# Optimization experiments

Measured on AMD Instinct MI355X. Metric: run time of the kernel, lower is better.

The kernel has to match this reference:

```python
import jax, jax.numpy as jnp
import numpy as np
from jax import lax

BN_EPS = 1e-5


def fps(xyz, n_group):
    """Farthest point sampling. xyz: (B,N,3) -> indices (B,n_group)."""
    B, N, _ = xyz.shape

    def step(carry, _):
        dist, far = carry                                   # (B,N), (B,)
        c = jnp.take_along_axis(xyz, far[:, None, None], axis=1)  # (B,1,3)
        d = jnp.sum((xyz - c) ** 2, axis=-1)                # (B,N)
        dist = jnp.minimum(dist, d)
        return (dist, jnp.argmax(dist, axis=-1).astype(jnp.int32)), far

    init = (jnp.full((B, N), 1e10, xyz.dtype), jnp.zeros((B,), jnp.int32))
    _, idxs = lax.scan(step, init, None, length=n_group)
    return jnp.swapaxes(idxs, 0, 1)                         # (B,n_group)


def knn_point(k, xyz, center):
    """k nearest neighbors of each center in xyz. -> idx (B,G,k)."""
    # squared distances (B,G,N), expanded-cdist form
    d = (jnp.sum(center ** 2, -1)[:, :, None]
         + jnp.sum(xyz ** 2, -1)[:, None, :]
         - 2.0 * jnp.einsum('bgc,bnc->bgn', center, xyz))
    _, idx = lax.top_k(-d, k)                               # smallest distances
    return idx


def batchnorm(x, gamma, beta):
    """Training-mode BatchNorm1d over (M, n) per channel. x: (M,n,C)."""
    mu = jnp.mean(x, axis=(0, 1))
    var = jnp.var(x, axis=(0, 1))
    return (x - mu) * lax.rsqrt(var + BN_EPS) * gamma + beta


def encoder(pg, W1, b1, g1, be1, W2, b2, W3, b3, g2, be2, W4, b4):
    """PointNet encoder. pg: (B,G,n,3) -> (B,G,C)."""
    B, G, n, _ = pg.shape
    x = pg.reshape(B * G, n, 3)
    f = jnp.einsum('mnc,oc->mno', x, W1) + b1               # (M,n,128)
    f = jax.nn.relu(batchnorm(f, g1, be1))
    f = jnp.einsum('mnc,oc->mno', f, W2) + b2               # (M,n,256)
    fg = jnp.max(f, axis=1, keepdims=True)                  # (M,1,256)
    f = jnp.concatenate([jnp.broadcast_to(fg, f.shape), f], axis=-1)  # (M,n,512)
    f = jnp.einsum('mnc,oc->mno', f, W3) + b3               # (M,n,512)
    f = jax.nn.relu(batchnorm(f, g2, be2))
    f = jnp.einsum('mnc,oc->mno', f, W4) + b4               # (M,n,C)
    return jnp.max(f, axis=1).reshape(B, G, -1)


def setup_inputs() -> dict:
    key = jax.random.key(0)
    ks = jax.random.split(key, 8)
    C = 128
    xyz = jax.random.normal(ks[0], (16, 8192, 3), jnp.float32)
    s = 0.02
    return {
        'xyz': xyz,
        'W1': jax.random.normal(ks[1], (128, 3), jnp.float32) * s,
        'b1': jnp.zeros((128,), jnp.float32),
        'g1': jnp.ones((128,), jnp.float32),
        'be1': jnp.zeros((128,), jnp.float32),
        'W2': jax.random.normal(ks[2], (256, 128), jnp.float32) * s,
        'b2': jnp.zeros((256,), jnp.float32),
        'W3': jax.random.normal(ks[3], (512, 512), jnp.float32) * s,
        'b3': jnp.zeros((512,), jnp.float32),
        'g2': jnp.ones((512,), jnp.float32),
        'be2': jnp.zeros((512,), jnp.float32),
        'W4': jax.random.normal(ks[4], (C, 512), jnp.float32) * s,
        'b4': jnp.zeros((C,), jnp.float32),
        'n_group': 512,
    }


def reference(xyz, W1, b1, g1, be1, W2, b2, W3, b3, g2, be2, W4, b4, n_group):
    k = 32
    B, N, _ = xyz.shape
    cidx = fps(xyz, n_group)                                # (B,G)
    center = jnp.take_along_axis(xyz, cidx[:, :, None], axis=1)  # (B,G,3)
    idx = knn_point(k, xyz, center)                         # (B,G,k)
    # gather neighborhoods
    neighborhood = jnp.take_along_axis(
        xyz, idx.reshape(B, n_group * k)[:, :, None], axis=1
    ).reshape(B, n_group, k, 3)
    features = encoder(neighborhood, W1, b1, g1, be1, W2, b2, W3, b3, g2, be2, W4, b4)
    return center, features
```

## Files before the change

kernel.cpp:

```cpp
#include <hip/hip_runtime.h>

typedef unsigned short ushortT;
typedef unsigned int uintT;
typedef unsigned long long u64T;
typedef __bf16 bf16x8 __attribute__((ext_vector_type(8)));
typedef float f32x4 __attribute__((ext_vector_type(4)));

#define B_ 16
#define N_ 8192
#define G_ 512
#define KNN_ 32
#define M_ (B_*G_)
#define R_ (M_*KNN_)

static __device__ __forceinline__ ushortT f2bf(float f){
  uintT u = __float_as_uint(f);
  return (ushortT)((u + 0x7fffu + ((u >> 16) & 1u)) >> 16);
}
static __device__ __forceinline__ float bf2f(ushortT h){ return __uint_as_float(((uintT)h) << 16); }

union U16 { uint4 u; ushortT s[8]; bf16x8 v; };

#define SWZ_MAX(vv, pat) {                                              \
    uintT lo_ = (uintT)(vv), hi_ = (uintT)((vv) >> 32);                 \
    uintT olo_ = (uintT)__builtin_amdgcn_ds_swizzle((int)lo_, (pat));   \
    uintT ohi_ = (uintT)__builtin_amdgcn_ds_swizzle((int)hi_, (pat));   \
    u64T o_ = ((u64T)ohi_ << 32) | olo_;                                \
    (vv) = (o_ > (vv)) ? o_ : (vv); }

__global__ __launch_bounds__(512) void fps_kernel(const float* __restrict__ xyz,
                                                  float* __restrict__ center){
  const int b = blockIdx.x;
  const int tid = threadIdx.x;
  const float* P = xyz + (size_t)b * N_ * 3;
  __shared__ float sx[N_], sy[N_], sz[N_];
  __shared__ u64T slot[2][8];
  float px[16], py[16], pz[16], dist[16];
  uintT nI[16];
#pragma unroll
  for (int k = 0; k < 16; k++){
    int p = tid + (k << 9);
    float x = P[p*3+0], y = P[p*3+1], z = P[p*3+2];
    sx[p] = x; sy[p] = y; sz[p] = z;
    px[k] = x; py[k] = y; pz[k] = z;
    dist[k] = 1e10f;
    nI[k] = ~(uintT)p;
  }
  __syncthreads();
  const int lane = tid & 63, wv = tid >> 6;
  int far = 0;
  for (int s = 0; s < G_; s++){
    const float cx = sx[far], cy = sy[far], cz = sz[far];
    if (tid == 0){
      float* co = center + ((size_t)b * G_ + s) * 3;
      co[0] = cx; co[1] = cy; co[2] = cz;
    }
    u64T pk[16];
#pragma unroll
    for (int k = 0; k < 16; k++){
      float d0 = __fsub_rn(px[k], cx), d1 = __fsub_rn(py[k], cy), d2 = __fsub_rn(pz[k], cz);
      float d  = __fadd_rn(__fadd_rn(__fmul_rn(d0,d0), __fmul_rn(d1,d1)), __fmul_rn(d2,d2));
      float dd = fminf(dist[k], d);
      dist[k] = dd;
      pk[k] = ((u64T)__float_as_uint(dd) << 32) | nI[k];
    }
#pragma unroll
    for (int st = 8; st >= 1; st >>= 1)
#pragma unroll
      for (int k = 0; k < st; k++)
        pk[k] = (pk[k + st] > pk[k]) ? pk[k + st] : pk[k];
    u64T best = pk[0];
    SWZ_MAX(best, 0x041F)
    SWZ_MAX(best, 0x081F)
    SWZ_MAX(best, 0x101F)
    SWZ_MAX(best, 0x201F)
    SWZ_MAX(best, 0x401F)
    {
      u64T o = __shfl_xor(best, 32);
      best = (o > best) ? o : best;
    }
    if (lane == 0) slot[s & 1][wv] = best;
    __syncthreads();
    u64T v = slot[s & 1][lane & 7];
    SWZ_MAX(v, 0x041F)
    SWZ_MAX(v, 0x081F)
    SWZ_MAX(v, 0x101F)
    far = (int)(~(uintT)v) & (N_ - 1);
  }
}

__global__ __launch_bounds__(256) void knn_kernel(const float* __restrict__ xyz,
                                                  const float* __restrict__ center,
                                                  int* __restrict__ knnIdx){
  const int mc = blockIdx.x;
  const int b  = mc >> 9;
  const int tid = threadIdx.x;
  const int lane = tid & 63, w = tid >> 6;
  const float* P = xyz + (size_t)b * N_ * 3;
  const float cx = center[mc*3+0], cy = center[mc*3+1], cz = center[mc*3+2];
  const float tc = __fadd_rn(__fadd_rn(__fmul_rn(cx,cx), __fmul_rn(cy,cy)), __fmul_rn(cz,cz));
  uintT key[32];
  uintT bd = 0xFFFFFFFFu; int bk = 0;
#pragma unroll
  for (int k = 0; k < 32; k++){
    int p = tid + (k << 8);
    float x = P[p*3+0], y = P[p*3+1], z = P[p*3+2];
    float tx  = __fadd_rn(__fadd_rn(__fmul_rn(x,x), __fmul_rn(y,y)), __fmul_rn(z,z));
    float dot = __fadd_rn(__fadd_rn(__fmul_rn(cx,x), __fmul_rn(cy,y)), __fmul_rn(cz,z));
    float d   = __fsub_rn(__fadd_rn(tc, tx), __fmul_rn(2.0f, dot));
    uintT bb  = __float_as_uint(d);
    uintT kk  = bb ^ ((uintT)((int)bb >> 31) | 0x80000000u);
    key[k] = kk;
    if (kk < bd){ bd = kk; bk = k; }
  }
  __shared__ u64T sKeys[128];
  for (int r = 0; r < KNN_; r++){
    u64T me = ((u64T)bd << 32) | (uintT)(tid + (bk << 8));
    u64T m = me;
#pragma unroll
    for (int msk = 32; msk >= 1; msk >>= 1){
      u64T o = __shfl_xor(m, msk);
      m = (o < m) ? o : m;
    }
    if (lane == 0) sKeys[w * 32 + r] = m;
    if (me == m){
      uintT nb = 0xFFFFFFFFu; int nk = 0;
#pragma unroll
      for (int k = 0; k < 32; k++){
        uintT vv = (k == bk) ? 0xFFFFFFFFu : key[k];
        key[k] = vv;
        if (vv < nb){ nb = vv; nk = k; }
      }
      bd = nb; bk = nk;
    }
  }
  __syncthreads();
  if (w == 0){
    u64T e0 = sKeys[lane], e1 = sKeys[lane + 64];
    for (int r = 0; r < KNN_; r++){
      u64T be = (e0 < e1) ? e0 : e1;
      u64T m = be;
#pragma unroll
      for (int msk = 32; msk >= 1; msk >>= 1){
        u64T o = __shfl_xor(m, msk);
        m = (o < m) ? o : m;
      }
      if (lane == 0) knnIdx[(size_t)mc * KNN_ + r] = (int)(uintT)m;
      if (be == m){
        if (e0 == m) e0 = ~0ull; else e1 = ~0ull;
      }
    }
  }
}

__global__ __launch_bounds__(256) void moments_kernel(const float* __restrict__ xyz,
                                                      const int* __restrict__ knnIdx,
                                                      float* __restrict__ Mpart){
  const int t = threadIdx.x, blk = blockIdx.x;
  float m[9];
#pragma unroll
  for (int k = 0; k < 9; k++) m[k] = 0.f;
  for (int i = 0; i < 4; i++){
    int row = blk * 1024 + i * 256 + t;
    int p = knnIdx[row];
    int b = row >> 14;
    const float* pt = xyz + ((size_t)(b * N_ + p)) * 3;
    float x = pt[0], y = pt[1], z = pt[2];
    m[0]+=x; m[1]+=y; m[2]+=z; m[3]+=x*x; m[4]+=y*y; m[5]+=z*z; m[6]+=x*y; m[7]+=x*z; m[8]+=y*z;
  }
  __shared__ float red[4][9];
  const int lane = t & 63, w = t >> 6;
#pragma unroll
  for (int k = 0; k < 9; k++){
    float v = m[k];
#pragma unroll
    for (int sh = 32; sh >= 1; sh >>= 1) v += __shfl_xor(v, sh);
    if (lane == 0) red[w][k] = v;
  }
  __syncthreads();
  if (t < 9) Mpart[blk * 9 + t] = red[0][t] + red[1][t] + red[2][t] + red[3][t];
}

__global__ __launch_bounds__(128) void prep1_kernel(const float* __restrict__ Mpart,
                                                    const float* __restrict__ W1,
                                                    const float* __restrict__ b1,
                                                    const float* __restrict__ g1,
                                                    const float* __restrict__ be1,
                                                    float4* __restrict__ F1c){
  __shared__ float S[9];
  const int t = threadIdx.x;
  if (t < 9){
    float s = 0.f;
    for (int i = 0; i < 256; i++) s += Mpart[i * 9 + t];
    S[t] = s;
  }
  __syncthreads();
  const float invN = 1.0f / (float)R_;
  float mx = S[0]*invN, my = S[1]*invN, mz = S[2]*invN;
  float Cxx = S[3]*invN - mx*mx, Cyy = S[4]*invN - my*my, Czz = S[5]*invN - mz*mz;
  float Cxy = S[6]*invN - mx*my, Cxz = S[7]*invN - mx*mz, Cyz = S[8]*invN - my*mz;
  const int ch = t;
  float w0 = W1[ch*3+0], w1 = W1[ch*3+1], w2 = W1[ch*3+2], bb = b1[ch];
  float var = w0*w0*Cxx + w1*w1*Cyy + w2*w2*Czz + 2.f*(w0*w1*Cxy + w0*w2*Cxz + w1*w2*Cyz);
  float mu  = w0*mx + w1*my + w2*mz + bb;
  float sc  = rsqrtf(var + 1e-5f) * g1[ch];
  float sh  = be1[ch] - mu * sc;
  F1c[ch] = make_float4(w0*sc, w1*sc, w2*sc, fmaf(bb, sc, sh));
}

__global__ __launch_bounds__(256) void cast3_kernel(const float* __restrict__ W2,
                                                    const float* __restrict__ W3,
                                                    const float* __restrict__ W4,
                                                    ushortT* W2b, ushortT* W3b, ushortT* W4b){
  int i = blockIdx.x * 256 + threadIdx.x;
  if (i < 32768)  W2b[i] = f2bf(W2[i]);
  if (i < 262144) W3b[i] = f2bf(W3[i]);
  if (i < 65536)  W4b[i] = f2bf(W4[i]);
}

static __device__ __forceinline__ void a1_frags(const float* __restrict__ xyz,
                                                const int* __restrict__ knnIdx,
                                                const float4* __restrict__ F1c,
                                                int row, int lg, bf16x8 fr[4]){
  const int p = knnIdx[row];
  const int b = row >> 14;
  const float* pt = xyz + ((size_t)(b * N_ + p)) * 3;
  const float x = pt[0], y = pt[1], z = pt[2];
#pragma unroll
  for (int s = 0; s < 4; s++){
    U16 u;
#pragma unroll
    for (int j = 0; j < 8; j++){
      const float4 f = F1c[s * 32 + lg * 8 + j];
      const float h = fmaxf(fmaf(x, f.x, fmaf(y, f.y, fmaf(z, f.z, f.w))), 0.f);
      u.s[j] = f2bf(h);
    }
    fr[s] = u.v;
  }
}

__global__ __launch_bounds__(256) void f2g_kernel(const float* __restrict__ xyz,
                                                  const int* __restrict__ knnIdx,
                                                  const float4* __restrict__ F1c,
                                                  const ushortT* __restrict__ W2bf,
                                                  const float* __restrict__ b2,
                                                  ushortT* __restrict__ fg){
  const int rc = blockIdx.x;
  const int t = threadIdx.x, lane = t & 63, w = t >> 6;
  const int lr = lane & 15, lg = lane >> 4;
  const int row = rc * 64 + w * 16 + lr;
  bf16x8 a1[4];
  a1_frags(xyz, knnIdx, F1c, row, lg, a1);
  f32x4 acc[16];
#pragma unroll
  for (int c = 0; c < 16; c++) acc[c] = (f32x4){0.f,0.f,0.f,0.f};
#pragma unroll
  for (int s = 0; s < 4; s++)
#pragma unroll
    for (int ct = 0; ct < 16; ct++){
      bf16x8 bb = *reinterpret_cast<const bf16x8*>(W2bf + (size_t)(ct*16+lr)*128 + s*32 + lg*8);
      acc[ct] = __builtin_amdgcn_mfma_f32_16x16x32_bf16(a1[s], bb, acc[ct], 0, 0, 0);
    }
  __shared__ float wmax[4][256];
#pragma unroll
  for (int ct = 0; ct < 16; ct++){
    float cmax = fmaxf(fmaxf(acc[ct][0], acc[ct][1]), fmaxf(acc[ct][2], acc[ct][3]));
    cmax = fmaxf(cmax, __shfl_xor(cmax, 16));
    cmax = fmaxf(cmax, __shfl_xor(cmax, 32));
    if (lg == 0) wmax[w][ct*16+lr] = cmax;
  }
  __syncthreads();
  {
    float bb = b2[t];
    fg[((size_t)rc*2 + 0)*256 + t] = f2bf(fmaxf(wmax[0][t], wmax[1][t]) + bb);
    fg[((size_t)rc*2 + 1)*256 + t] = f2bf(fmaxf(wmax[2][t], wmax[3][t]) + bb);
  }
}

__global__ __launch_bounds__(512) void enc2s_kernel(const float* __restrict__ xyz,
                                                    const int* __restrict__ knnIdx,
                                                    const float4* __restrict__ F1c,
                                                    const ushortT* __restrict__ W2bf,
                                                    const float* __restrict__ b2,
                                                    ushortT* __restrict__ fg,
                                                    float* __restrict__ fgsum,
                                                    ushortT* __restrict__ S2g){
  __shared__ ushortT sS2[128 * 256];
  __shared__ float wmax[8][256];
  __shared__ float wsum[8][256];
  const int blk = blockIdx.x;
  const int t = threadIdx.x, lane = t & 63, wv = t >> 6;
  const int lr = lane & 15, lg = lane >> 4;
  bf16x8 a1[4];
  a1_frags(xyz, knnIdx, F1c, blk*128 + wv*16 + lr, lg, a1);
  f32x4 acc[16];
#pragma unroll
  for (int c = 0; c < 16; c++) acc[c] = (f32x4){0.f,0.f,0.f,0.f};
#pragma unroll
  for (int s = 0; s < 4; s++)
#pragma unroll
    for (int ct = 0; ct < 16; ct++){
      bf16x8 bb = *reinterpret_cast<const bf16x8*>(W2bf + (size_t)(ct*16+lr)*128 + s*32 + lg*8);
      acc[ct] = __builtin_amdgcn_mfma_f32_16x16x32_bf16(a1[s], bb, acc[ct], 0, 0, 0);
    }
#pragma unroll
  for (int ct = 0; ct < 16; ct++){
    const int col = ct*16 + lr;
    const float bb = b2[col];
    float cmax = -3.0e38f, csum = 0.f;
#pragma unroll
    for (int i = 0; i < 4; i++){
      int row = wv*16 + lg*4 + i;
      ushortT sv = f2bf(acc[ct][i] + bb);
      sS2[row*256 + (col ^ ((row & 7) << 3))] = sv;
      csum += bf2f(sv);
      cmax = fmaxf(cmax, acc[ct][i]);
    }
    cmax = fmaxf(cmax, __shfl_xor(cmax, 16));
    cmax = fmaxf(cmax, __shfl_xor(cmax, 32));
    csum += __shfl_xor(csum, 16); csum += __shfl_xor(csum, 32);
    if (lg == 0){ wmax[wv][col] = cmax; wsum[wv][col] = csum; }
  }
  __syncthreads();
#pragma unroll
  for (int q = 0; q < 2; q++){
    int gl = q*2 + (t >> 8);
    int col = t & 255;
    float bb = b2[col];
    fg   [((size_t)blk*4 + gl)*256 + col] = f2bf(fmaxf(wmax[2*gl][col], wmax[2*gl+1][col]) + bb);
    fgsum[((size_t)blk*4 + gl)*256 + col] = wsum[2*gl][col] + wsum[2*gl+1][col];
  }
  const uint4* src = reinterpret_cast<const uint4*>(sS2);
  uint4* dst = reinterpret_cast<uint4*>(S2g + (size_t)blk * 32768);
#pragma unroll
  for (int i = 0; i < 8; i++) dst[t + i*512] = src[t + i*512];
}

__global__ __launch_bounds__(256) void u_kernel(const ushortT* __restrict__ fg,
                                                const ushortT* __restrict__ W3bf,
                                                const float* __restrict__ b3,
                                                float* __restrict__ U){
  const int bid = blockIdx.x;
  const int rc = bid >> 2, cc = bid & 3;
  const int t = threadIdx.x, lane = t & 63, w = t >> 6;
  const int lr = lane & 15, lg = lane >> 4;
  const int arow = rc * 64 + w * 16 + lr;
  f32x4 acc[8];
#pragma unroll
  for (int c = 0; c < 8; c++) acc[c] = (f32x4){0.f,0.f,0.f,0.f};
#pragma unroll
  for (int s = 0; s < 8; s++){
    bf16x8 a = *reinterpret_cast<const bf16x8*>(fg + (size_t)arow*256 + s*32 + lg*8);
#pragma unroll
    for (int ct = 0; ct < 8; ct++){
      bf16x8 bb = *reinterpret_cast<const bf16x8*>(W3bf + (size_t)(cc*128+ct*16+lr)*512 + s*32 + lg*8);
      acc[ct] = __builtin_amdgcn_mfma_f32_16x16x32_bf16(a, bb, acc[ct], 0, 0, 0);
    }
  }
#pragma unroll
  for (int ct = 0; ct < 8; ct++){
    int col = cc*128 + ct*16 + lr;
    float bb = b3[col];
#pragma unroll
    for (int i = 0; i < 4; i++){
      int crow = rc*64 + w*16 + lg*4 + i;
      U[(size_t)crow * 512 + col] = acc[ct][i] + bb;
    }
  }
}

__global__ __launch_bounds__(256) void v_kernel(const float* __restrict__ fgsum,
                                                const ushortT* __restrict__ W3bf,
                                                const float* __restrict__ U,
                                                float* __restrict__ UVpart){
  const int bid = blockIdx.x;
  const int rc = bid >> 2, cc = bid & 3;
  const int t = threadIdx.x, lane = t & 63, w = t >> 6;
  const int lr = lane & 15, lg = lane >> 4;
  const int arow = rc * 64 + w * 16 + lr;
  f32x4 acc[8];
#pragma unroll
  for (int c = 0; c < 8; c++) acc[c] = (f32x4){0.f,0.f,0.f,0.f};
#pragma unroll
  for (int s = 0; s < 8; s++){
    int kk = s*32 + lg*8;
    float4 fa = *reinterpret_cast<const float4*>(&fgsum[(size_t)arow*256 + kk]);
    float4 fb = *reinterpret_cast<const float4*>(&fgsum[(size_t)arow*256 + kk + 4]);
    U16 ua;
    ua.s[0]=f2bf(fa.x); ua.s[1]=f2bf(fa.y); ua.s[2]=f2bf(fa.z); ua.s[3]=f2bf(fa.w);
    ua.s[4]=f2bf(fb.x); ua.s[5]=f2bf(fb.y); ua.s[6]=f2bf(fb.z); ua.s[7]=f2bf(fb.w);
#pragma unroll
    for (int ct = 0; ct < 8; ct++){
      bf16x8 bb = *reinterpret_cast<const bf16x8*>(W3bf + (size_t)(cc*128+ct*16+lr)*512 + 256 + kk);
      acc[ct] = __builtin_amdgcn_mfma_f32_16x16x32_bf16(ua.v, bb, acc[ct], 0, 0, 0);
    }
  }
  __shared__ float sUV[4][128];
#pragma unroll
  for (int ct = 0; ct < 8; ct++){
    int col = cc*128 + ct*16 + lr;
    float uv = 0.f;
#pragma unroll
    for (int i = 0; i < 4; i++){
      int g = rc*64 + w*16 + lg*4 + i;
      uv += acc[ct][i] * U[(size_t)g * 512 + col];
    }
    uv += __shfl_xor(uv, 16); uv += __shfl_xor(uv, 32);
    if (lg == 0) sUV[w][ct*16+lr] = uv;
  }
  __syncthreads();
  if (t < 128)
    UVpart[(size_t)rc * 512 + cc*128 + t] = sUV[0][t] + sUV[1][t] + sUV[2][t] + sUV[3][t];
}

__global__ __launch_bounds__(512) void gram2_kernel(const ushortT* __restrict__ S2g,
                                                    float* __restrict__ Gpart,
                                                    int tilesPerBlk){
  __shared__ ushortT sT[256 * 136];
  const int blk = blockIdx.x;
  const int t = threadIdx.x, lane = t & 63, wv = t >> 6;
  const int lr = lane & 15, lg = lane >> 4;
  f32x4 gacc[32];
#pragma unroll
  for (int c = 0; c < 32; c++) gacc[c] = (f32x4){0.f,0.f,0.f,0.f};
  const int r  = t >> 2;
  const int cb = (t & 3) * 64;
  for (int tile = 0; tile < tilesPerBlk; tile++){
    const int rt = blk * tilesPerBlk + tile;
    __syncthreads();
    const int swz = (r & 7) << 3;
#pragma unroll
    for (int u4 = 0; u4 < 8; u4++){
      int sc0 = cb + u4*8;
      U16 raw; raw.u = *reinterpret_cast<const uint4*>(S2g + (size_t)rt*32768 + r*256 + sc0);
      int tc0 = sc0 ^ swz;
#pragma unroll
      for (int j = 0; j < 8; j++)
        sT[(tc0 + j)*136 + r] = raw.s[j];
    }
    __syncthreads();
#pragma unroll
    for (int ks = 0; ks < 4; ks++){
      const int k0 = ks*32 + lg*8;
      bf16x8 aA[2];
#pragma unroll
      for (int ii = 0; ii < 2; ii++)
        aA[ii] = *reinterpret_cast<const bf16x8*>(&sT[((2*wv+ii)*16 + lr)*136 + k0]);
#pragma unroll
      for (int j = 0; j < 16; j++){
        bf16x8 bB = *reinterpret_cast<const bf16x8*>(&sT[(j*16 + lr)*136 + k0]);
        gacc[0*16+j] = __builtin_amdgcn_mfma_f32_16x16x32_bf16(aA[0], bB, gacc[0*16+j], 0,0,0);
        gacc[1*16+j] = __builtin_amdgcn_mfma_f32_16x16x32_bf16(aA[1], bB, gacc[1*16+j], 0,0,0);
      }
    }
  }
  float* Gp = Gpart + (size_t)blk * 65536;
#pragma unroll
  for (int ii = 0; ii < 2; ii++)
#pragma unroll
    for (int j = 0; j < 16; j++)
#pragma unroll
      for (int i = 0; i < 4; i++){
        int ci = (2*wv + ii)*16 + lg*4 + i;
        int cj = j*16 + lr;
        Gp[ci*256 + cj] = gacc[ii*16+j][i];
      }
}

__global__ __launch_bounds__(256) void gred_kernel(const float* __restrict__ Gpart,
                                                   float* __restrict__ G, int nPart){
  int i = blockIdx.x * 256 + threadIdx.x;
  float s = 0.f;
  for (int b = 0; b < nPart; b++) s += Gpart[(size_t)b * 65536 + i];
  G[i] = s;
}

__global__ __launch_bounds__(256) void ured_kernel(const float* __restrict__ U,
                                                   const float* __restrict__ fgsum,
                                                   float* __restrict__ Upart,
                                                   float* __restrict__ Usqpart,
                                                   float* __restrict__ CSpart){
  const int blk = blockIdx.x;
  const int slice = blk >> 3, part = blk & 7;
  const int t = threadIdx.x;
  {
    const int cl = t & 63, gsub = t >> 6;
    const int c = part*64 + cl;
    float su = 0.f, sq = 0.f;
    for (int g = slice*1024 + gsub; g < slice*1024 + 1024; g += 4){
      float u = U[(size_t)g * 512 + c];
      su += u; sq += u*u;
    }
    __shared__ float rU[4][64], rQ[4][64];
    rU[gsub][cl] = su; rQ[gsub][cl] = sq;
    __syncthreads();
    if (t < 64){
      Upart  [(size_t)slice*512 + part*64 + t] = rU[0][t]+rU[1][t]+rU[2][t]+rU[3][t];
      Usqpart[(size_t)slice*512 + part*64 + t] = rQ[0][t]+rQ[1][t]+rQ[2][t]+rQ[3][t];
    }
  }
  __syncthreads();
  {
    const int cl = t & 31, gsub = t >> 5;
    const int c2 = part*32 + cl;
    float cs = 0.f;
    for (int g = slice*1024 + gsub; g < slice*1024 + 1024; g += 8)
      cs += fgsum[(size_t)g * 256 + c2];
    __shared__ float rC[8][32];
    rC[gsub][cl] = cs;
    __syncthreads();
    if (t < 32){
      float s = 0.f;
#pragma unroll
      for (int k = 0; k < 8; k++) s += rC[k][t];
      CSpart[(size_t)slice*256 + part*32 + t] = s;
    }
  }
}

__global__ __launch_bounds__(256) void fin2_kernel(const float* __restrict__ G,
                                                   const float* __restrict__ CSpart,
                                                   const float* __restrict__ Upart,
                                                   const float* __restrict__ Usqpart,
                                                   const float* __restrict__ UVpart,
                                                   const ushortT* __restrict__ W3bf,
                                                   const float* __restrict__ g2,
                                                   const float* __restrict__ be2,
                                                   float* __restrict__ scale2,
                                                   float* __restrict__ shift2){
  const int blk = blockIdx.x, t = threadIdx.x;
  __shared__ float sw[256];
  __shared__ float r1[4], r2[4], r3[4];
  float csf = 0.f;
#pragma unroll
  for (int s = 0; s < 8; s++) csf += CSpart[s*256 + t];
  for (int sub = 0; sub < 4; sub++){
    const int c = blk*4 + sub;
    sw[t] = bf2f(W3bf[(size_t)c*512 + 256 + t]);
    __syncthreads();
    const float wj = sw[t];
    float dot = 0.f;
    const float* Grow = G + (size_t)t * 256;
    for (int k = 0; k < 256; k++) dot += sw[k] * Grow[k];
    float quad = wj * dot;
    float cdot = wj * csf;
    float uvv  = (t < 128) ? UVpart[(size_t)t * 512 + c] : 0.f;
    float a = quad, bq = cdot, cq = uvv;
#pragma unroll
    for (int m = 32; m >= 1; m >>= 1){
      a  += __shfl_xor(a, m); bq += __shfl_xor(bq, m); cq += __shfl_xor(cq, m);
    }
    if ((t & 63) == 0){ r1[t>>6] = a; r2[t>>6] = bq; r3[t>>6] = cq; }
    __syncthreads();
    if (t == 0){
      float wGw  = r1[0]+r1[1]+r1[2]+r1[3];
      float csw  = r2[0]+r2[1]+r2[2]+r2[3];
      float sUV  = r3[0]+r3[1]+r3[2]+r3[3];
      float sU = 0.f, sQ = 0.f;
#pragma unroll
      for (int s = 0; s < 8; s++){
        sU += Upart  [s*512 + c];
        sQ += Usqpart[s*512 + c];
      }
      const float invN = 1.0f / (float)R_;
      float mu = (csw + 32.f * sU) * invN;
      float e2 = (wGw + 2.f * sUV + 32.f * sQ) * invN;
      float var = e2 - mu * mu;
      float sc = rsqrtf(var + 1e-5f) * g2[c];
      scale2[c] = sc;
      shift2[c] = be2[c] - mu * sc;
    }
    __syncthreads();
  }
}

static __device__ __forceinline__ void phaseA_s2(const float* __restrict__ xyz,
                                                 const int* __restrict__ knnIdx,
                                                 const float4* __restrict__ F1c,
                                                 const ushortT* __restrict__ W2bf,
                                                 const float* __restrict__ b2,
                                                 ushortT* sS2, int blk,
                                                 int wv, int lr, int lg){
  bf16x8 a1[4];
  a1_frags(xyz, knnIdx, F1c, blk*128 + wv*16 + lr, lg, a1);
  f32x4 acc[16];
#pragma unroll
  for (int c = 0; c < 16; c++) acc[c] = (f32x4){0.f,0.f,0.f,0.f};
#pragma unroll
  for (int s = 0; s < 4; s++)
#pragma unroll
    for (int ct = 0; ct < 16; ct++){
      bf16x8 bb = *reinterpret_cast<const bf16x8*>(W2bf + (size_t)(ct*16+lr)*128 + s*32 + lg*8);
      acc[ct] = __builtin_amdgcn_mfma_f32_16x16x32_bf16(a1[s], bb, acc[ct], 0, 0, 0);
    }
#pragma unroll
  for (int ct = 0; ct < 16; ct++){
    int col = ct*16 + lr;
    float bb = b2[col];
#pragma unroll
    for (int i = 0; i < 4; i++){
      int row = wv*16 + lg*4 + i;
      sS2[row*256 + (col ^ ((row & 7) << 3))] = f2bf(acc[ct][i] + bb);
    }
  }
}

#define PHASE2(PASS, ACC)                                                               \
  {                                                                                     \
    _Pragma("unroll")                                                                   \
    for (int s = 0; s < 8; s++){                                                        \
      const int kk = s*32 + lg*8;                                                       \
      bf16x8 b0 = *reinterpret_cast<const bf16x8*>(                                     \
          W3bf + (size_t)((PASS)*256 + wv*32 + 0 + lr)*512 + 256 + kk);                 \
      bf16x8 b1 = *reinterpret_cast<const bf16x8*>(                                     \
          W3bf + (size_t)((PASS)*256 + wv*32 + 16 + lr)*512 + 256 + kk);                \
      _Pragma("unroll")                                                                 \
      for (int rf = 0; rf < 8; rf++){                                                   \
        int row = rf*16 + lr;                                                           \
        bf16x8 a = *reinterpret_cast<const bf16x8*>(                                    \
            &sS2[row*256 + (kk ^ ((row & 7) << 3))]);                                   \
        ACC[rf][0] = __builtin_amdgcn_mfma_f32_16x16x32_bf16(a, b0, ACC[rf][0], 0,0,0); \
        ACC[rf][1] = __builtin_amdgcn_mfma_f32_16x16x32_bf16(a, b1, ACC[rf][1], 0,0,0); \
      }                                                                                 \
    }                                                                                   \
  }

__global__ __launch_bounds__(512) void enc3_kernel(const float* __restrict__ xyz,
                                                   const int* __restrict__ knnIdx,
                                                   const float4* __restrict__ F1c,
                                                   const ushortT* __restrict__ W2bf,
                                                   const float* __restrict__ b2,
                                                   const ushortT* __restrict__ W3bf,
                                                   const float* __restrict__ U,
                                                   float* __restrict__ P2sum,
                                                   float* __restrict__ P2sq){
  __shared__ ushortT sS2[128 * 256];
  const int blk = blockIdx.x;
  const int t = threadIdx.x, lane = t & 63, wv = t >> 6;
  const int lr = lane & 15, lg = lane >> 4;
  phaseA_s2(xyz, knnIdx, F1c, W2bf, b2, sS2, blk, wv, lr, lg);
  __syncthreads();
#pragma unroll
  for (int pass = 0; pass < 2; pass++){
    f32x4 acc[8][2];
#pragma unroll
    for (int rf = 0; rf < 8; rf++){ acc[rf][0] = (f32x4){0,0,0,0}; acc[rf][1] = (f32x4){0,0,0,0}; }
    PHASE2(pass, acc)
#pragma unroll
    for (int ct = 0; ct < 2; ct++){
      int col = pass*256 + wv*32 + ct*16 + lr;
      float s = 0.f, q = 0.f;
#pragma unroll
      for (int rf = 0; rf < 8; rf++){
        float uv = U[(size_t)(blk*4 + (rf >> 1)) * 512 + col];
#pragma unroll
        for (int i = 0; i < 4; i++){
          float v = acc[rf][ct][i] + uv;
          s += v; q += v * v;
        }
      }
      s += __shfl_xor(s, 16); s += __shfl_xor(s, 32);
      q += __shfl_xor(q, 16); q += __shfl_xor(q, 32);
      if (lg == 0){
        P2sum[(size_t)blk * 512 + col] = s;
        P2sq [(size_t)blk * 512 + col] = q;
      }
    }
  }
}

__global__ __launch_bounds__(256) void fin_kernel(const float* __restrict__ Psum,
                                                  const float* __restrict__ Psq,
                                                  int nPart, int C, float invN,
                                                  const float* __restrict__ g,
                                                  const float* __restrict__ be,
                                                  float* __restrict__ scale,
                                                  float* __restrict__ shift){
  const int ch = blockIdx.x, t = threadIdx.x;
  float s = 0.f, q = 0.f;
  for (int i = t; i < nPart; i += 256){
    s += Psum[(size_t)i * C + ch];
    q += Psq [(size_t)i * C + ch];
  }
  __shared__ float ls[4], lq[4];
#pragma unroll
  for (int m = 32; m >= 1; m >>= 1){ s += __shfl_xor(s, m); q += __shfl_xor(q, m); }
  if ((t & 63) == 0){ ls[t >> 6] = s; lq[t >> 6] = q; }
  __syncthreads();
  if (t == 0){
    s = ls[0] + ls[1] + ls[2] + ls[3];
    q = lq[0] + lq[1] + lq[2] + lq[3];
    float mu = s * invN;
    float var = q * invN - mu * mu;
    float sc = rsqrtf(var + 1e-5f) * g[ch];
    scale[ch] = sc;
    shift[ch] = be[ch] - mu * sc;
  }
}

#define ENC4_BODY                                                                       \
  f32x4 acc0[8][2], acc1[8][2];                                                         \
  _Pragma("unroll")                                                                     \
  for (int rf = 0; rf < 8; rf++){                                                       \
    acc0[rf][0] = (f32x4){0,0,0,0}; acc0[rf][1] = (f32x4){0,0,0,0};                     \
    acc1[rf][0] = (f32x4){0,0,0,0}; acc1[rf][1] = (f32x4){0,0,0,0};                     \
  }                                                                                     \
  PHASE2(0, acc0)                                                                       \
  PHASE2(1, acc1)                                                                       \
  __syncthreads();                                                                      \
  f32x4 accF[8];                                                                        \
  _Pragma("unroll")                                                                     \
  for (int rf = 0; rf < 8; rf++) accF[rf] = (f32x4){0,0,0,0};                           \
  _Pragma("unroll")                                                                     \
  for (int ct = 0; ct < 2; ct++){                                                       \
    int colh = wv*32 + ct*16 + lr;                                                      \
    _Pragma("unroll")                                                                   \
    for (int rf = 0; rf < 8; rf++){                                                     \
      float uv = U[(size_t)(blk*4 + (rf >> 1)) * 512 + colh];                           \
      _Pragma("unroll")                                                                 \
      for (int i = 0; i < 4; i++){                                                      \
        int row = rf*16 + lg*4 + i;                                                     \
        float v = acc0[rf][ct][i] + uv;                                                 \
        sS2[row*256 + (colh ^ ((row & 7) << 3))] =                                      \
            f2bf(fmaxf(fmaf(v, s_sc[colh], s_sh[colh]), 0.f));                          \
      }                                                                                 \
    }                                                                                   \
  }                                                                                     \
  __syncthreads();                                                                      \
  _Pragma("unroll")                                                                     \
  for (int s = 0; s < 8; s++){                                                          \
    const int kk = s*32 + lg*8;                                                         \
    bf16x8 b = *reinterpret_cast<const bf16x8*>(W4bf + (size_t)(wv*16 + lr)*512 + kk);  \
    _Pragma("unroll")                                                                   \
    for (int rf = 0; rf < 8; rf++){                                                     \
      int row = rf*16 + lr;                                                             \
      bf16x8 a = *reinterpret_cast<const bf16x8*>(&sS2[row*256 + (kk ^ ((row & 7) << 3))]); \
      accF[rf] = __builtin_amdgcn_mfma_f32_16x16x32_bf16(a, b, accF[rf], 0, 0, 0);      \
    }                                                                                   \
  }                                                                                     \
  __syncthreads();                                                                      \
  _Pragma("unroll")                                                                     \
  for (int ct = 0; ct < 2; ct++){                                                       \
    int colh = wv*32 + ct*16 + lr;                                                      \
    int col  = 256 + colh;                                                              \
    _Pragma("unroll")                                                                   \
    for (int rf = 0; rf < 8; rf++){                                                     \
      float uv = U[(size_t)(blk*4 + (rf >> 1)) * 512 + col];                            \
      _Pragma("unroll")                                                                 \
      for (int i = 0; i < 4; i++){                                                      \
        int row = rf*16 + lg*4 + i;                                                     \
        float v = acc1[rf][ct][i] + uv;                                                 \
        sS2[row*256 + (colh ^ ((row & 7) << 3))] =                                      \
            f2bf(fmaxf(fmaf(v, s_sc[col], s_sh[col]), 0.f));                            \
      }                                                                                 \
    }                                                                                   \
  }                                                                                     \
  __syncthreads();                                                                      \
  _Pragma("unroll")                                                                     \
  for (int s = 0; s < 8; s++){                                                          \
    const int kk = s*32 + lg*8;                                                         \
    bf16x8 b = *reinterpret_cast<const bf16x8*>(W4bf + (size_t)(wv*16 + lr)*512 + 256 + kk); \
    _Pragma("unroll")                                                                   \
    for (int rf = 0; rf < 8; rf++){                                                     \
      int row = rf*16 + lr;                                                             \
      bf16x8 a = *reinterpret_cast<const bf16x8*>(&sS2[row*256 + (kk ^ ((row & 7) << 3))]); \
      accF[rf] = __builtin_amdgcn_mfma_f32_16x16x32_bf16(a, b, accF[rf], 0, 0, 0);      \
    }                                                                                   \
  }                                                                                     \
  const float bb4 = b4[wv*16 + lr];                                                     \
  _Pragma("unroll")                                                                     \
  for (int gl = 0; gl < 4; gl++){                                                       \
    float m = -3.0e38f;                                                                 \
    _Pragma("unroll")                                                                   \
    for (int i = 0; i < 4; i++){                                                        \
      m = fmaxf(m, accF[2*gl    ][i]);                                                  \
      m = fmaxf(m, accF[2*gl + 1][i]);                                                  \
    }                                                                                   \
    m = fmaxf(m, __shfl_xor(m, 16));                                                    \
    m = fmaxf(m, __shfl_xor(m, 32));                                                    \
    if (lg == 0)                                                                        \
      feat[((size_t)blk*4 + gl)*128 + wv*16 + lr] = m + bb4;                            \
  }

__global__ __launch_bounds__(512) void enc4_kernel(const float* __restrict__ xyz,
                                                   const int* __restrict__ knnIdx,
                                                   const float4* __restrict__ F1c,
                                                   const ushortT* __restrict__ W2bf,
                                                   const float* __restrict__ b2,
                                                   const ushortT* __restrict__ W3bf,
                                                   const float* __restrict__ U,
                                                   const float* __restrict__ scale2,
                                                   const float* __restrict__ shift2,
                                                   const ushortT* __restrict__ W4bf,
                                                   const float* __restrict__ b4,
                                                   float* __restrict__ feat){
  __shared__ ushortT sS2[128 * 256];
  __shared__ float s_sc[512], s_sh[512];
  const int blk = blockIdx.x;
  const int t = threadIdx.x, lane = t & 63, wv = t >> 6;
  const int lr = lane & 15, lg = lane >> 4;
  if (t < 512){ s_sc[t] = scale2[t]; s_sh[t] = shift2[t]; }
  phaseA_s2(xyz, knnIdx, F1c, W2bf, b2, sS2, blk, wv, lr, lg);
  __syncthreads();
  ENC4_BODY
}

__global__ __launch_bounds__(512) void enc4r_kernel(const ushortT* __restrict__ S2g,
                                                    const ushortT* __restrict__ W3bf,
                                                    const float* __restrict__ U,
                                                    const float* __restrict__ scale2,
                                                    const float* __restrict__ shift2,
                                                    const ushortT* __restrict__ W4bf,
                                                    const float* __restrict__ b4,
                                                    float* __restrict__ feat){
  __shared__ ushortT sS2[128 * 256];
  __shared__ float s_sc[512], s_sh[512];
  const int blk = blockIdx.x;
  const int t = threadIdx.x, lane = t & 63, wv = t >> 6;
  const int lr = lane & 15, lg = lane >> 4;
  if (t < 512){ s_sc[t] = scale2[t]; s_sh[t] = shift2[t]; }
  {
    const uint4* src = reinterpret_cast<const uint4*>(S2g + (size_t)blk * 32768);
    uint4* dst = reinterpret_cast<uint4*>(sS2);
#pragma unroll
    for (int i = 0; i < 8; i++) dst[t + i*512] = src[t + i*512];
  }
  __syncthreads();
  ENC4_BODY
}

extern "C" void kernel_launch(void* const* d_in, const int* in_sizes, int n_in,
                              void* d_out, int out_size, void* d_ws, size_t ws_size,
                              hipStream_t stream){
  const float* xyz = (const float*)d_in[0];
  const float* W1  = (const float*)d_in[1];
  const float* b1  = (const float*)d_in[2];
  const float* g1  = (const float*)d_in[3];
  const float* be1 = (const float*)d_in[4];
  const float* W2  = (const float*)d_in[5];
  const float* b2  = (const float*)d_in[6];
  const float* W3  = (const float*)d_in[7];
  const float* b3  = (const float*)d_in[8];
  const float* g2  = (const float*)d_in[9];
  const float* be2 = (const float*)d_in[10];
  const float* W4  = (const float*)d_in[11];
  const float* b4  = (const float*)d_in[12];

  float* out = (float*)d_out;
  float* center = out;
  float* feat   = out + (size_t)B_ * G_ * 3;

  char* p = (char*)d_ws;
  size_t used = 0;
  auto alloc = [&](size_t bytes) -> char* {
    char* r = p + used; used += (bytes + 255) & ~(size_t)255; return r;
  };
  int*     knnIdx = (int*)    alloc((size_t)R_ * 4);
  ushortT* W2bf   = (ushortT*)alloc(32768 * 2);
  ushortT* W3bf   = (ushortT*)alloc(262144 * 2);
  ushortT* W4bf   = (ushortT*)alloc(65536 * 2);
  float4*  F1c    = (float4*) alloc(128 * 16);
  float*   Mpart  = (float*)  alloc(256 * 9 * 4);
  ushortT* fg     = (ushortT*)alloc((size_t)M_ * 256 * 2);
  float*   U      = (float*)  alloc((size_t)M_ * 512 * 4);
  float*   scale2 = (float*)  alloc(512 * 4);
  float*   shift2 = (float*)  alloc(512 * 4);

  const size_t s2_b    = (size_t)R_ * 256 * 2;
  const size_t fgsum_b = (size_t)M_ * 256 * 4;
  const size_t small_b = (256*1024) + (256*1024) + (64*1024);
  const size_t margin  = 4u << 20;
  int NBG = 0;
  if      (ws_size >= used + s2_b + fgsum_b + small_b + (size_t)256*65536*4 + margin) NBG = 256;
  else if (ws_size >= used + s2_b + fgsum_b + small_b + (size_t)128*65536*4 + margin) NBG = 128;
  else if (ws_size >= used + s2_b + fgsum_b + small_b + (size_t)64 *65536*4 + margin) NBG = 64;

  cast3_kernel  <<<dim3(1024), dim3(256),  0, stream>>>(W2, W3, W4, W2bf, W3bf, W4bf);
  fps_kernel    <<<dim3(B_),   dim3(512),  0, stream>>>(xyz, center);
  knn_kernel    <<<dim3(M_),   dim3(256),  0, stream>>>(xyz, center, knnIdx);
  moments_kernel<<<dim3(256),  dim3(256),  0, stream>>>(xyz, knnIdx, Mpart);
  prep1_kernel  <<<dim3(1),    dim3(128),  0, stream>>>(Mpart, W1, b1, g1, be1, F1c);

  if (NBG){
    float*   fgsum   = (float*)  alloc(fgsum_b);
    ushortT* S2g     = (ushortT*)alloc(s2_b);
    float*   UVpart  = (float*)  alloc(128 * 512 * 4);
    float*   G       = (float*)  alloc(65536 * 4);
    float*   Upart   = (float*)  alloc(8 * 512 * 4);
    float*   Usqpart = (float*)  alloc(8 * 512 * 4);
    float*   CSpart  = (float*)  alloc(8 * 256 * 4);
    float*   Gpart   = (float*)  alloc((size_t)NBG * 65536 * 4);
    enc2s_kernel<<<dim3(2048), dim3(512), 0, stream>>>(xyz, knnIdx, F1c, W2bf, b2, fg, fgsum, S2g);
    u_kernel    <<<dim3(512),  dim3(256), 0, stream>>>(fg, W3bf, b3, U);
    v_kernel    <<<dim3(512),  dim3(256), 0, stream>>>(fgsum, W3bf, U, UVpart);
    gram2_kernel<<<dim3(NBG),  dim3(512), 0, stream>>>(S2g, Gpart, 2048/NBG);
    gred_kernel <<<dim3(256),  dim3(256), 0, stream>>>(Gpart, G, NBG);
    ured_kernel <<<dim3(64),   dim3(256), 0, stream>>>(U, fgsum, Upart, Usqpart, CSpart);
    fin2_kernel <<<dim3(128),  dim3(256), 0, stream>>>(G, CSpart, Upart, Usqpart, UVpart,
                                                       W3bf, g2, be2, scale2, shift2);
    enc4r_kernel<<<dim3(2048), dim3(512), 0, stream>>>(S2g, W3bf, U, scale2, shift2, W4bf, b4, feat);
  } else {
    float* P2sum = (float*)alloc((size_t)2048 * 512 * 4);
    float* P2sq  = (float*)alloc((size_t)2048 * 512 * 4);
    f2g_kernel <<<dim3(4096), dim3(256), 0, stream>>>(xyz, knnIdx, F1c, W2bf, b2, fg);
    u_kernel   <<<dim3(512),  dim3(256), 0, stream>>>(fg, W3bf, b3, U);
    enc3_kernel<<<dim3(2048), dim3(512), 0, stream>>>(xyz, knnIdx, F1c, W2bf, b2, W3bf, U, P2sum, P2sq);
    fin_kernel <<<dim3(512),  dim3(256), 0, stream>>>(P2sum, P2sq, 2048, 512, 1.0f/(float)R_,
                                                      g2, be2, scale2, shift2);
    enc4_kernel<<<dim3(2048), dim3(512), 0, stream>>>(xyz, knnIdx, F1c, W2bf, b2, W3bf, U,
                                                      scale2, shift2, W4bf, b4, feat);
  }
}
```

Before: 1.554 ms.

## Use packed FP32 math and split float/index argmax reduction in FPS

```diff
diff --git a/kernel.cpp b/kernel.cpp
--- a/kernel.cpp
+++ b/kernel.cpp
@@ -21,12 +21,32 @@
 
 union U16 { uint4 u; ushortT s[8]; bf16x8 v; };
 
+static __device__ __forceinline__ float2 pk_add(float2 a, float2 b){
+  float2 d;
+  asm("v_pk_add_f32 %0, %1, %2" : "=v"(d) : "v"(a), "v"(b));
+  return d;
+}
+static __device__ __forceinline__ float2 pk_mul(float2 a, float2 b){
+  float2 d;
+  asm("v_pk_mul_f32 %0, %1, %2" : "=v"(d) : "v"(a), "v"(b));
+  return d;
+}
+
 #define SWZ_MAX(vv, pat) {                                              \
     uintT lo_ = (uintT)(vv), hi_ = (uintT)((vv) >> 32);                 \
     uintT olo_ = (uintT)__builtin_amdgcn_ds_swizzle((int)lo_, (pat));   \
     uintT ohi_ = (uintT)__builtin_amdgcn_ds_swizzle((int)hi_, (pat));   \
     u64T o_ = ((u64T)ohi_ << 32) | olo_;                                \
     (vv) = (o_ > (vv)) ? o_ : (vv); }
+
+#define SWZF_MAX(vv, pat) {                                                          \
+    float o_ = __uint_as_float((uintT)__builtin_amdgcn_ds_swizzle(                   \
+        (int)__float_as_uint(vv), (pat)));                                           \
+    (vv) = fmaxf((vv), o_); }
+
+#define SWZU_MAX(vv, pat) {                                                          \
+    uintT o_ = (uintT)__builtin_amdgcn_ds_swizzle((int)(vv), (pat));                 \
+    (vv) = ((o_ > (vv)) ? o_ : (vv)); }
 
 __global__ __launch_bounds__(512) void fps_kernel(const float* __restrict__ xyz,
                                                   float* __restrict__ center){
@@ -35,16 +55,22 @@
   const float* P = xyz + (size_t)b * N_ * 3;
   __shared__ float sx[N_], sy[N_], sz[N_];
   __shared__ u64T slot[2][8];
-  float px[16], py[16], pz[16], dist[16];
+  float2 px[8], py[8], pz[8], dist[8];
   uintT nI[16];
 #pragma unroll
-  for (int k = 0; k < 16; k++){
-    int p = tid + (k << 9);
-    float x = P[p*3+0], y = P[p*3+1], z = P[p*3+2];
-    sx[p] = x; sy[p] = y; sz[p] = z;
-    px[k] = x; py[k] = y; pz[k] = z;
-    dist[k] = 1e10f;
-    nI[k] = ~(uintT)p;
+  for (int k = 0; k < 8; k++){
+    int p0 = tid + ((2*k    ) << 9);
+    int p1 = tid + ((2*k + 1) << 9);
+    float x0 = P[p0*3+0], y0 = P[p0*3+1], z0 = P[p0*3+2];
+    float x1 = P[p1*3+0], y1 = P[p1*3+1], z1 = P[p1*3+2];
+    sx[p0] = x0; sy[p0] = y0; sz[p0] = z0;
+    sx[p1] = x1; sy[p1] = y1; sz[p1] = z1;
+    px[k] = make_float2(x0, x1);
+    py[k] = make_float2(y0, y1);
+    pz[k] = make_float2(z0, z1);
+    dist[k] = make_float2(1e10f, 1e10f);
+    nI[2*k    ] = ~(uintT)p0;
+    nI[2*k + 1] = ~(uintT)p1;
   }
   __syncthreads();
   const int lane = tid & 63, wv = tid >> 6;
@@ -55,30 +81,43 @@
       float* co = center + ((size_t)b * G_ + s) * 3;
       co[0] = cx; co[1] = cy; co[2] = cz;
     }
-    u64T pk[16];
-#pragma unroll
-    for (int k = 0; k < 16; k++){
-      float d0 = __fsub_rn(px[k], cx), d1 = __fsub_rn(py[k], cy), d2 = __fsub_rn(pz[k], cz);
-      float d  = __fadd_rn(__fadd_rn(__fmul_rn(d0,d0), __fmul_rn(d1,d1)), __fmul_rn(d2,d2));
-      float dd = fminf(dist[k], d);
-      dist[k] = dd;
-      pk[k] = ((u64T)__float_as_uint(dd) << 32) | nI[k];
-    }
-#pragma unroll
-    for (int st = 8; st >= 1; st >>= 1)
-#pragma unroll
-      for (int k = 0; k < st; k++)
-        pk[k] = (pk[k + st] > pk[k]) ? pk[k + st] : pk[k];
-    u64T best = pk[0];
-    SWZ_MAX(best, 0x041F)
-    SWZ_MAX(best, 0x081F)
-    SWZ_MAX(best, 0x101F)
-    SWZ_MAX(best, 0x201F)
-    SWZ_MAX(best, 0x401F)
-    {
-      u64T o = __shfl_xor(best, 32);
-      best = (o > best) ? o : best;
-    }
+    const float2 ncx = make_float2(-cx, -cx);
+    const float2 ncy = make_float2(-cy, -cy);
+    const float2 ncz = make_float2(-cz, -cz);
+#pragma unroll
+    for (int k = 0; k < 8; k++){
+      float2 dx = pk_add(px[k], ncx);
+      float2 dy = pk_add(py[k], ncy);
+      float2 dz = pk_add(pz[k], ncz);
+      float2 d  = pk_add(pk_add(pk_mul(dx, dx), pk_mul(dy, dy)), pk_mul(dz, dz));
+      dist[k] = make_float2(fminf(dist[k].x, d.x), fminf(dist[k].y, d.y));
+    }
+    float m0 = fmaxf(fmaxf(dist[0].x, dist[0].y), fmaxf(dist[1].x, dist[1].y));
+    float m1 = fmaxf(fmaxf(dist[2].x, dist[2].y), fmaxf(dist[3].x, dist[3].y));
+    float m2 = fmaxf(fmaxf(dist[4].x, dist[4].y), fmaxf(dist[5].x, dist[5].y));
+    float m3 = fmaxf(fmaxf(dist[6].x, dist[6].y), fmaxf(dist[7].x, dist[7].y));
+    float bv = fmaxf(fmaxf(m0, m1), fmaxf(m2, m3));
+    SWZF_MAX(bv, 0x041F)
+    SWZF_MAX(bv, 0x081F)
+    SWZF_MAX(bv, 0x101F)
+    SWZF_MAX(bv, 0x201F)
+    SWZF_MAX(bv, 0x401F)
+    { float o = __shfl_xor(bv, 32); bv = fmaxf(bv, o); }
+    uintT cand = 0;
+#pragma unroll
+    for (int k = 0; k < 8; k++){
+      uintT c0 = (dist[k].x == bv) ? nI[2*k]     : 0u;
+      uintT c1 = (dist[k].y == bv) ? nI[2*k + 1] : 0u;
+      uintT cm = (c0 > c1) ? c0 : c1;
+      cand = (cm > cand) ? cm : cand;
+    }
+    SWZU_MAX(cand, 0x041F)
+    SWZU_MAX(cand, 0x081F)
+    SWZU_MAX(cand, 0x101F)
+    SWZU_MAX(cand, 0x201F)
+    SWZU_MAX(cand, 0x401F)
+    { uintT o = __shfl_xor(cand, 32); cand = (o > cand) ? o : cand; }
+    u64T best = ((u64T)__float_as_uint(bv) << 32) | cand;
     if (lane == 0) slot[s & 1][wv] = best;
     __syncthreads();
     u64T v = slot[s & 1][lane & 7];
```

New measurement: 1.666 ms. +7.2%, slower.

## Fuse two W3 GEMM passes into one with 64-column tiles per wave

Applied to the files above, without the earlier changes.

```diff
diff --git a/kernel.cpp b/kernel.cpp
--- a/kernel.cpp
+++ b/kernel.cpp
@@ -625,6 +625,29 @@
     }                                                                                   \
   }
 
+#define PHASE2F(ACC)                                                                    \
+  {                                                                                     \
+    _Pragma("unroll")                                                                   \
+    for (int s = 0; s < 8; s++){                                                        \
+      const int kk = s*32 + lg*8;                                                       \
+      bf16x8 bbf[4];                                                                    \
+      _Pragma("unroll")                                                                 \
+      for (int ct = 0; ct < 4; ct++)                                                    \
+        bbf[ct] = *reinterpret_cast<const bf16x8*>(                                     \
+            W3bf + (size_t)(wv*64 + ct*16 + lr)*512 + 256 + kk);                        \
+      _Pragma("unroll")                                                                 \
+      for (int rf = 0; rf < 8; rf++){                                                   \
+        int row = rf*16 + lr;                                                           \
+        bf16x8 a = *reinterpret_cast<const bf16x8*>(                                    \
+            &sS2[row*256 + (kk ^ ((row & 7) << 3))]);                                   \
+        ACC[rf][0] = __builtin_amdgcn_mfma_f32_16x16x32_bf16(a, bbf[0], ACC[rf][0], 0,0,0); \
+        ACC[rf][1] = __builtin_amdgcn_mfma_f32_16x16x32_bf16(a, bbf[1], ACC[rf][1], 0,0,0); \
+        ACC[rf][2] = __builtin_amdgcn_mfma_f32_16x16x32_bf16(a, bbf[2], ACC[rf][2], 0,0,0); \
+        ACC[rf][3] = __builtin_amdgcn_mfma_f32_16x16x32_bf16(a, bbf[3], ACC[rf][3], 0,0,0); \
+      }                                                                                 \
+    }                                                                                   \
+  }
+
 __global__ __launch_bounds__(512) void enc3_kernel(const float* __restrict__ xyz,
                                                    const int* __restrict__ knnIdx,
                                                    const float4* __restrict__ F1c,
@@ -699,30 +722,32 @@
 }
 
 #define ENC4_BODY                                                                       \
-  f32x4 acc0[8][2], acc1[8][2];                                                         \
+  f32x4 acc[8][4];                                                                      \
   _Pragma("unroll")                                                                     \
   for (int rf = 0; rf < 8; rf++){                                                       \
-    acc0[rf][0] = (f32x4){0,0,0,0}; acc0[rf][1] = (f32x4){0,0,0,0};                     \
-    acc1[rf][0] = (f32x4){0,0,0,0}; acc1[rf][1] = (f32x4){0,0,0,0};                     \
+    acc[rf][0] = (f32x4){0,0,0,0}; acc[rf][1] = (f32x4){0,0,0,0};                       \
+    acc[rf][2] = (f32x4){0,0,0,0}; acc[rf][3] = (f32x4){0,0,0,0};                       \
   }                                                                                     \
-  PHASE2(0, acc0)                                                                       \
-  PHASE2(1, acc1)                                                                       \
-  __syncthreads();                                                                      \
+  PHASE2F(acc)                                                                          \
+  __syncthreads();                                       \
   f32x4 accF[8];                                                                        \
   _Pragma("unroll")                                                                     \
   for (int rf = 0; rf < 8; rf++) accF[rf] = (f32x4){0,0,0,0};                           \
-  _Pragma("unroll")                                                                     \
-  for (int ct = 0; ct < 2; ct++){                                                       \
-    int colh = wv*32 + ct*16 + lr;                                                      \
+                                        \
+  if (wv < 4){                                                                          \
     _Pragma("unroll")                                                                   \
-    for (int rf = 0; rf < 8; rf++){                                                     \
-      float uv = U[(size_t)(blk*4 + (rf >> 1)) * 512 + colh];                           \
+    for (int ct = 0; ct < 4; ct++){                                                     \
+      int col = wv*64 + ct*16 + lr;                                                     \
       _Pragma("unroll")                                                                 \
-      for (int i = 0; i < 4; i++){                                                      \
-        int row = rf*16 + lg*4 + i;                                                     \
-        float v = acc0[rf][ct][i] + uv;                                                 \
-        sS2[row*256 + (colh ^ ((row & 7) << 3))] =                                      \
-            f2bf(fmaxf(fmaf(v, s_sc[colh], s_sh[colh]), 0.f));                          \
+      for (int rf = 0; rf < 8; rf++){                                                   \
+        float uv = U[(size_t)(blk*4 + (rf >> 1)) * 512 + col];                          \
+        _Pragma("unroll")                                                               \
+        for (int i = 0; i < 4; i++){                                                    \
+          int row = rf*16 + lg*4 + i;                                                   \
+          float v = acc[rf][ct][i] + uv;                                                \
+          sS2[row*256 + (col ^ ((row & 7) << 3))] =                                     \
+              f2bf(fmaxf(fmaf(v, s_sc[col], s_sh[col]), 0.f));                          \
+        }                                                                               \
       }                                                                                 \
     }                                                                                   \
   }                                                                                     \
@@ -739,19 +764,22 @@
     }                                                                                   \
   }                                                                                     \
   __syncthreads();                                                                      \
-  _Pragma("unroll")                                                                     \
-  for (int ct = 0; ct < 2; ct++){                                                       \
-    int colh = wv*32 + ct*16 + lr;                                                      \
-    int col  = 256 + colh;                                                              \
+                                      \
+  if (wv >= 4){                                                                         \
     _Pragma("unroll")                                                                   \
-    for (int rf = 0; rf < 8; rf++){                                                     \
-      float uv = U[(size_t)(blk*4 + (rf >> 1)) * 512 + col];                            \
+    for (int ct = 0; ct < 4; ct++){                                                     \
+      int col  = wv*64 + ct*16 + lr;                                      \
+      int coll = col - 256;                                                             \
       _Pragma("unroll")                                                                 \
-      for (int i = 0; i < 4; i++){                                                      \
-        int row = rf*16 + lg*4 + i;                                                     \
-        float v = acc1[rf][ct][i] + uv;                                                 \
-        sS2[row*256 + (colh ^ ((row & 7) << 3))] =                                      \
-            f2bf(fmaxf(fmaf(v, s_sc[col], s_sh[col]), 0.f));                            \
+      for (int rf = 0; rf < 8; rf++){                                                   \
+        float uv = U[(size_t)(blk*4 + (rf >> 1)) * 512 + col];                          \
+        _Pragma("unroll")                                                               \
+        for (int i = 0; i < 4; i++){                                                    \
+          int row = rf*16 + lg*4 + i;                                                   \
+          float v = acc[rf][ct][i] + uv;                                                \
+          sS2[row*256 + (coll ^ ((row & 7) << 3))] =                                    \
+              f2bf(fmaxf(fmaf(v, s_sc[col], s_sh[col]), 0.f));                          \
+        }                                                                               \
       }                                                                                 \
     }                                                                                   \
   }                                                                                     \
```

Result: no change. 1.569 ms (+0.9%).
